# Performance work log

Measured on AMD Instinct MI355X. Metric: run time of the kernel, lower is better.

Reference implementation:

```python
import jax, jax.numpy as jnp
import numpy as np

N_NODES = 100000
N_HID = 128
N_ETYPES = 10
N_EDGES = 100000  # edges per etype


def setup_inputs() -> dict:
    key = jax.random.key(0)
    k1, k2, k3, k4 = jax.random.split(key, 4)
    h = jax.random.normal(k1, (N_NODES, N_HID), dtype=jnp.float32)
    W = jax.random.normal(k2, (N_ETYPES, N_HID), dtype=jnp.float32)
    src = jax.random.randint(k3, (N_ETYPES, N_EDGES), 0, N_NODES, dtype=jnp.int64)
    dst = jax.random.randint(k4, (N_ETYPES, N_EDGES), 0, N_NODES, dtype=jnp.int64)
    rel = jnp.arange(N_ETYPES, dtype=jnp.int64)  # rel2idx: etype -> relation row
    return {"h": h, "W": W, "src": src, "dst": dst, "rel": rel}


def reference(h, W, src, dst, rel):
    # DistMult: score(e) = sum_d h[src_e, d] * W[rel_e, d] * h[dst_e, d]
    h_u = h[src]          # [T, E, d]  gather src features
    h_v = h[dst]          # [T, E, d]  gather dst features
    h_r = W[rel]          # [T, d]     relation embedding per etype
    scores = jnp.einsum('ted,td,ted->te', h_u, h_r, h_v)  # [T, E]
    # pretrain_mode path applies sigmoid per etype
    return jax.nn.sigmoid(scores)
```

## Files before the change

### kernel.cpp

```cpp
#include <hip/hip_runtime.h>
#include <hip/hip_fp16.h>
#include <math.h>

#define N_NODES  100000
#define N_HID    128
#define N_ETYPES 10
#define N_EDGES  100000
#define TOT_EDGES (N_ETYPES * N_EDGES)

#define NSLICE    64
#define SLICE_CAP 16384
#define EPB_SC    2048

#define EDGES_PER_HW 4

typedef __attribute__((ext_vector_type(2))) _Float16 h2v;

#if defined(__has_builtin)
#if __has_builtin(__builtin_amdgcn_fdot2)
#define HAVE_FDOT2 1
#endif
#endif

__device__ __forceinline__ float dot2acc(h2v a, h2v b, float c) {
#ifdef HAVE_FDOT2
    return __builtin_amdgcn_fdot2(a, b, c, false);
#else
    return c + (float)a.x * (float)b.x + (float)a.y * (float)b.y;
#endif
}

template<int CTRL>
__device__ __forceinline__ float ror_add(float p) {
    int r = __builtin_amdgcn_update_dpp(0, __float_as_int(p), CTRL, 0xF, 0xF, true);
    return p + __int_as_float(r);
}
__device__ __forceinline__ float row16_sum(float p) {
    p = ror_add<0x121>(p);
    p = ror_add<0x122>(p);
    p = ror_add<0x124>(p);
    p = ror_add<0x128>(p);
    return p;
}

__device__ __forceinline__ float dot_row(uint4 a, uint4 b, uint4 w) {
    union { uint4 u; h2v p[4]; } ua, ub, uw;
    ua.u = a; ub.u = b; uw.u = w;
    float p = dot2acc(ua.p[0], (h2v)(uw.p[0] * ub.p[0]), 0.0f);
    p = dot2acc(ua.p[1], (h2v)(uw.p[1] * ub.p[1]), p);
    p = dot2acc(ua.p[2], (h2v)(uw.p[2] * ub.p[2]), p);
    p = dot2acc(ua.p[3], (h2v)(uw.p[3] * ub.p[3]), p);
    return p;
}

__global__ __launch_bounds__(256) void convert_kernel(
    const float* __restrict__ h, const float* __restrict__ W,
    const int*   __restrict__ rel,
    __half* __restrict__ h16, __half* __restrict__ Wr16,
    int* __restrict__ cursor)
{
    const size_t i = ((size_t)blockIdx.x * 256 + threadIdx.x) * 8;
    const float4 f0 = *(const float4*)(h + i);
    const float4 f1 = *(const float4*)(h + i + 4);
    union { uint4 u; __half2 p[4]; } pk;
    pk.p[0] = __floats2half2_rn(f0.x, f0.y);
    pk.p[1] = __floats2half2_rn(f0.z, f0.w);
    pk.p[2] = __floats2half2_rn(f1.x, f1.y);
    pk.p[3] = __floats2half2_rn(f1.z, f1.w);
    *(uint4*)(h16 + i) = pk.u;

    if (blockIdx.x == 0) {
        if (threadIdx.x < NSLICE) cursor[threadIdx.x] = threadIdx.x * SLICE_CAP;
        if (threadIdx.x < (N_ETYPES * N_HID / 8)) {
            const int j = threadIdx.x * 8;
            const int t = j >> 7;
            const int c = j & (N_HID - 1);
            const int r = rel[t];
            const float4 g0 = *(const float4*)(W + (size_t)r * N_HID + c);
            const float4 g1 = *(const float4*)(W + (size_t)r * N_HID + c + 4);
            union { uint4 u; __half2 p[4]; } pw;
            pw.p[0] = __floats2half2_rn(g0.x, g0.y);
            pw.p[1] = __floats2half2_rn(g0.z, g0.w);
            pw.p[2] = __floats2half2_rn(g1.x, g1.y);
            pw.p[3] = __floats2half2_rn(g1.z, g1.w);
            *(uint4*)(Wr16 + j) = pw.u;
        }
    }
}

__global__ __launch_bounds__(256) void scatter_kernel(
    const int* __restrict__ src, const int* __restrict__ dst,
    int* __restrict__ cursor, uint2* __restrict__ rec)
{
    __shared__ int lcnt[NSLICE];
    __shared__ int lbase[NSLICE];
    const int tid = threadIdx.x;
    if (tid < NSLICE) lcnt[tid] = 0;
    __syncthreads();

    const int e0 = blockIdx.x * EPB_SC + tid * 8;
    const bool active = (e0 < TOT_EDGES);

    int ss[8], dd[8], sl[8];
    if (active) {
        const int4 s0 = *(const int4*)(src + e0);
        const int4 s1 = *(const int4*)(src + e0 + 4);
        const int4 d0 = *(const int4*)(dst + e0);
        const int4 d1 = *(const int4*)(dst + e0 + 4);
        ss[0]=s0.x; ss[1]=s0.y; ss[2]=s0.z; ss[3]=s0.w;
        ss[4]=s1.x; ss[5]=s1.y; ss[6]=s1.z; ss[7]=s1.w;
        dd[0]=d0.x; dd[1]=d0.y; dd[2]=d0.z; dd[3]=d0.w;
        dd[4]=d1.x; dd[5]=d1.y; dd[6]=d1.z; dd[7]=d1.w;
        #pragma unroll
        for (int k = 0; k < 8; ++k) {
            sl[k] = (int)(((unsigned long long)(unsigned)dd[k] * 1407374884ULL) >> 41);
            atomicAdd(&lcnt[sl[k]], 1);
        }
    }
    __syncthreads();
    if (tid < NSLICE) {
        const int c = lcnt[tid];
        lbase[tid] = c ? atomicAdd(&cursor[tid], c) : 0;
        lcnt[tid] = 0;
    }
    __syncthreads();
    if (active) {
        #pragma unroll
        for (int k = 0; k < 8; ++k) {
            const int e   = e0 + k;
            const int ety = (int)(((unsigned long long)(unsigned)e * 1407374884ULL) >> 47);
            const int off = e - ety * N_EDGES;
            const int r   = atomicAdd(&lcnt[sl[k]], 1);
            const int pos = lbase[sl[k]] + r;
            const unsigned lo = (unsigned)ss[k] | ((unsigned)dd[k] << 17);
            const unsigned hi = ((unsigned)dd[k] >> 15) | ((unsigned)ety << 2) | ((unsigned)off << 6);
            rec[pos] = make_uint2(lo, hi);
        }
    }
}

__global__ __launch_bounds__(256) void score_kernel(
    const __half* __restrict__ h16,
    const __half* __restrict__ Wr16,
    const uint2*  __restrict__ rec,
    const int*    __restrict__ cursor,
    float*        __restrict__ out)
{
    const int tid  = threadIdx.x;
    const int lane = tid & 63;
    const int g    = lane >> 4;
    const int gl   = lane & 15;
    const int wid  = tid >> 6;

    const int b     = blockIdx.x;
    const int x     = b & 7;
    const int j     = b >> 3;
    const int s     = x + ((j >> 8) << 3);
    const int chunk = j & 255;
    const int sbase = s << 14;
    const int cnt   = cursor[s] - sbase;
    const int e_lo  = (chunk << 6) + (wid << 4);
    if (e_lo >= cnt) return;

    const unsigned col = (unsigned)gl << 3;

    const int i0 = e_lo + g;
    const int i1 = e_lo + 4 + g;
    const int i2 = e_lo + 8 + g;
    const int i3 = e_lo + 12 + g;
    const uint2 r0 = rec[sbase + (i0 < cnt ? i0 : 0)];
    const uint2 r1 = rec[sbase + (i1 < cnt ? i1 : 0)];
    const uint2 r2 = rec[sbase + (i2 < cnt ? i2 : 0)];
    const uint2 r3 = rec[sbase + (i3 < cnt ? i3 : 0)];

    const unsigned s0 = r0.x & 131071u, d0 = ((r0.x >> 17) | (r0.y << 15)) & 131071u;
    const unsigned t0 = (r0.y >> 2) & 15u,  o0 = r0.y >> 6;
    const unsigned s1 = r1.x & 131071u, d1 = ((r1.x >> 17) | (r1.y << 15)) & 131071u;
    const unsigned t1 = (r1.y >> 2) & 15u,  o1 = r1.y >> 6;
    const unsigned s2 = r2.x & 131071u, d2 = ((r2.x >> 17) | (r2.y << 15)) & 131071u;
    const unsigned t2 = (r2.y >> 2) & 15u,  o2 = r2.y >> 6;
    const unsigned s3 = r3.x & 131071u, d3 = ((r3.x >> 17) | (r3.y << 15)) & 131071u;
    const unsigned t3 = (r3.y >> 2) & 15u,  o3 = r3.y >> 6;

    const uint4 Wv0 = *(const uint4*)(Wr16 + ((t0 << 7) + col));
    const uint4 Wv1 = *(const uint4*)(Wr16 + ((t1 << 7) + col));
    const uint4 Wv2 = *(const uint4*)(Wr16 + ((t2 << 7) + col));
    const uint4 Wv3 = *(const uint4*)(Wr16 + ((t3 << 7) + col));
    const uint4 A0 = *(const uint4*)(h16 + ((s0 << 7) + col));
    const uint4 B0 = *(const uint4*)(h16 + ((d0 << 7) + col));
    const uint4 A1 = *(const uint4*)(h16 + ((s1 << 7) + col));
    const uint4 B1 = *(const uint4*)(h16 + ((d1 << 7) + col));
    const uint4 A2 = *(const uint4*)(h16 + ((s2 << 7) + col));
    const uint4 B2 = *(const uint4*)(h16 + ((d2 << 7) + col));
    const uint4 A3 = *(const uint4*)(h16 + ((s3 << 7) + col));
    const uint4 B3 = *(const uint4*)(h16 + ((d3 << 7) + col));

    float p0 = row16_sum(dot_row(A0, B0, Wv0));
    float p1 = row16_sum(dot_row(A1, B1, Wv1));
    float p2 = row16_sum(dot_row(A2, B2, Wv2));
    float p3 = row16_sum(dot_row(A3, B3, Wv3));

    if (gl < 4) {
        const int ii = e_lo + (gl << 2) + g;
        if (ii < cnt) {
            const float    res = (gl == 0) ? p0 : (gl == 1) ? p1 : (gl == 2) ? p2 : p3;
            const unsigned tt  = (gl == 0) ? t0 : (gl == 1) ? t1 : (gl == 2) ? t2 : t3;
            const unsigned oo  = (gl == 0) ? o0 : (gl == 1) ? o1 : (gl == 2) ? o2 : o3;
            out[tt * N_EDGES + oo] = 1.0f / (1.0f + __expf(-res));
        }
    }
}

__global__ __launch_bounds__(256) void convert_legacy_kernel(
    const float* __restrict__ h, const float* __restrict__ W,
    __half* __restrict__ h16, __half* __restrict__ W16)
{
    const size_t i = ((size_t)blockIdx.x * 256 + threadIdx.x) * 8;
    const float4 f0 = *(const float4*)(h + i);
    const float4 f1 = *(const float4*)(h + i + 4);
    union { uint4 u; __half2 p[4]; } pk;
    pk.p[0] = __floats2half2_rn(f0.x, f0.y);
    pk.p[1] = __floats2half2_rn(f0.z, f0.w);
    pk.p[2] = __floats2half2_rn(f1.x, f1.y);
    pk.p[3] = __floats2half2_rn(f1.z, f1.w);
    *(uint4*)(h16 + i) = pk.u;
    if (blockIdx.x == 0 && threadIdx.x < (N_ETYPES * N_HID / 8)) {
        const size_t j = (size_t)threadIdx.x * 8;
        const float4 g0 = *(const float4*)(W + j);
        const float4 g1 = *(const float4*)(W + j + 4);
        union { uint4 u; __half2 p[4]; } pw;
        pw.p[0] = __floats2half2_rn(g0.x, g0.y);
        pw.p[1] = __floats2half2_rn(g0.z, g0.w);
        pw.p[2] = __floats2half2_rn(g1.x, g1.y);
        pw.p[3] = __floats2half2_rn(g1.z, g1.w);
        *(uint4*)(W16 + j) = pw.u;
    }
}

__global__ __launch_bounds__(256) void distmult_score_f16_kernel(
    const __half* __restrict__ h16,
    const __half* __restrict__ W16,
    const int*    __restrict__ src,
    const int*    __restrict__ dst,
    const int*    __restrict__ rel,
    float*        __restrict__ out)
{
    const int t    = blockIdx.y;
    const int lane = threadIdx.x & 63;
    const int g    = lane >> 4;
    const int gl   = lane & 15;
    const int wid  = threadIdx.x >> 6;
    const int r = rel[t];
    union { uint4 u; h2v p[4]; } uw;
    uw.u = ((const uint4*)(W16 + (size_t)r * N_HID))[gl];
    const int base = t * N_EDGES;
    const int e0   = (blockIdx.x * 4 + wid) * 8;
    const int* sp = src + base + e0 + g;
    const int* dp = dst + base + e0 + g;
    const int s0 = sp[0], s1 = sp[4], d0 = dp[0], d1 = dp[4];
    const unsigned col = (unsigned)gl << 3;
    const uint4 A0 = *(const uint4*)(h16 + (((unsigned)s0 << 7) + col));
    const uint4 B0 = *(const uint4*)(h16 + (((unsigned)d0 << 7) + col));
    const uint4 A1 = *(const uint4*)(h16 + (((unsigned)s1 << 7) + col));
    const uint4 B1 = *(const uint4*)(h16 + (((unsigned)d1 << 7) + col));
    float p0 = row16_sum(dot_row(A0, B0, uw.u));
    float p1 = row16_sum(dot_row(A1, B1, uw.u));
    if (gl < 2) {
        const float res = gl ? p1 : p0;
        const int e = e0 + g + (gl << 2);
        out[base + e] = 1.0f / (1.0f + __expf(-res));
    }
}

__global__ __launch_bounds__(256) void distmult_score_f32_kernel(
    const float* __restrict__ h,
    const float* __restrict__ W,
    const int*   __restrict__ src,
    const int*   __restrict__ dst,
    const int*   __restrict__ rel,
    float*       __restrict__ out)
{
    const int t    = blockIdx.y;
    const int lane = threadIdx.x & 31;
    const int hw   = (blockIdx.x << 3) + (threadIdx.x >> 5);
    const int r = rel[t];
    const float4 w4 = ((const float4*)(W + (size_t)r * N_HID))[lane];
    const long base = (long)t * N_EDGES;
    const int  e0   = hw * EDGES_PER_HW;
    float res = 0.0f;
    #pragma unroll
    for (int k = 0; k < EDGES_PER_HW; ++k) {
        const int e = e0 + k;
        const int s = src[base + e];
        const int d = dst[base + e];
        const float4 a = ((const float4*)(h + (size_t)s * N_HID))[lane];
        const float4 b = ((const float4*)(h + (size_t)d * N_HID))[lane];
        float p = a.x * w4.x * b.x + a.y * w4.y * b.y
                + a.z * w4.z * b.z + a.w * w4.w * b.w;
        p += __shfl_xor(p, 16, 64);
        p += __shfl_xor(p, 8, 64);
        p += __shfl_xor(p, 4, 64);
        p += __shfl_xor(p, 2, 64);
        p += __shfl_xor(p, 1, 64);
        if (lane == k) res = p;
    }
    if (lane < EDGES_PER_HW) {
        out[base + e0 + lane] = 1.0f / (1.0f + __expf(-res));
    }
}

extern "C" void kernel_launch(void* const* d_in, const int* in_sizes, int n_in,
                              void* d_out, int out_size, void* d_ws, size_t ws_size,
                              hipStream_t stream) {
    const float* h   = (const float*)d_in[0];
    const float* W   = (const float*)d_in[1];
    const int*   src = (const int*)d_in[2];
    const int*   dst = (const int*)d_in[3];
    const int*   rel = (const int*)d_in[4];
    float*       out = (float*)d_out;

    const size_t h16_bytes  = (size_t)N_NODES * N_HID * sizeof(__half);
    const size_t wr16_bytes = 4096;
    const size_t rec_bytes  = (size_t)NSLICE * SLICE_CAP * 8;
    const size_t cur_bytes  = 4096;
    const size_t need_full  = h16_bytes + wr16_bytes + rec_bytes + cur_bytes;
    const size_t need_f16   = h16_bytes + (size_t)N_ETYPES * N_HID * sizeof(__half);

    if (ws_size >= need_full) {
        char* w = (char*)d_ws;
        __half* h16    = (__half*)w;   w += h16_bytes;
        __half* Wr16   = (__half*)w;   w += wr16_bytes;
        uint2*  rec    = (uint2*)w;    w += rec_bytes;
        int*    cursor = (int*)w;

        convert_kernel<<<(int)(((size_t)N_NODES * N_HID) / (256 * 8)), 256, 0, stream>>>(
            h, W, rel, h16, Wr16, cursor);
        scatter_kernel<<<(TOT_EDGES + EPB_SC - 1) / EPB_SC, 256, 0, stream>>>(
            src, dst, cursor, rec);
        score_kernel<<<NSLICE * (SLICE_CAP / 64), 256, 0, stream>>>(
            h16, Wr16, rec, cursor, out);
    } else if (ws_size >= need_f16) {
        __half* h16 = (__half*)d_ws;
        __half* W16 = h16 + (size_t)N_NODES * N_HID;
        convert_legacy_kernel<<<(int)(((size_t)N_NODES * N_HID) / (256 * 8)), 256, 0, stream>>>(
            h, W, h16, W16);
        dim3 grid(N_EDGES / 32, N_ETYPES);
        distmult_score_f16_kernel<<<grid, 256, 0, stream>>>(h16, W16, src, dst, rel, out);
    } else {
        dim3 grid(N_EDGES / (8 * EDGES_PER_HW), N_ETYPES);
        distmult_score_f32_kernel<<<grid, 256, 0, stream>>>(h, W, src, dst, rel, out);
    }
}
```

Baseline: 156.2 us.

## Fuse convert, scatter and score into one cooperative kernel with grid syncs

```diff
diff --git a/kernel.cpp b/kernel.cpp
--- a/kernel.cpp
+++ b/kernel.cpp
@@ -1,6 +1,9 @@
 #include <hip/hip_runtime.h>
+#include <hip/hip_cooperative_groups.h>
 #include <hip/hip_fp16.h>
 #include <math.h>
+
+namespace cg = cooperative_groups;
 
 #define N_NODES  100000
 #define N_HID    128
@@ -11,6 +14,9 @@
 #define NSLICE    64
 #define SLICE_CAP 16384
 #define EPB_SC    2048
+#define NBLK_SC   ((TOT_EDGES + EPB_SC - 1) / EPB_SC)
+#define NBFUSED   1024
+#define NVB_SCORE (NSLICE * (SLICE_CAP / 64))
 
 #define EDGES_PER_HW 4
 
@@ -53,52 +59,47 @@
     return p;
 }
 
-__global__ __launch_bounds__(256) void convert_kernel(
-    const float* __restrict__ h, const float* __restrict__ W,
-    const int*   __restrict__ rel,
-    __half* __restrict__ h16, __half* __restrict__ Wr16,
-    int* __restrict__ cursor)
-{
-    const size_t i = ((size_t)blockIdx.x * 256 + threadIdx.x) * 8;
-    const float4 f0 = *(const float4*)(h + i);
-    const float4 f1 = *(const float4*)(h + i + 4);
+
+__device__ __forceinline__ void conv_vec8(const float* __restrict__ h,
+                                          __half* __restrict__ h16, size_t off) {
+    const float4 f0 = *(const float4*)(h + off);
+    const float4 f1 = *(const float4*)(h + off + 4);
     union { uint4 u; __half2 p[4]; } pk;
     pk.p[0] = __floats2half2_rn(f0.x, f0.y);
     pk.p[1] = __floats2half2_rn(f0.z, f0.w);
     pk.p[2] = __floats2half2_rn(f1.x, f1.y);
     pk.p[3] = __floats2half2_rn(f1.z, f1.w);
-    *(uint4*)(h16 + i) = pk.u;
-
-    if (blockIdx.x == 0) {
-        if (threadIdx.x < NSLICE) cursor[threadIdx.x] = threadIdx.x * SLICE_CAP;
-        if (threadIdx.x < (N_ETYPES * N_HID / 8)) {
-            const int j = threadIdx.x * 8;
-            const int t = j >> 7;
-            const int c = j & (N_HID - 1);
-            const int r = rel[t];
-            const float4 g0 = *(const float4*)(W + (size_t)r * N_HID + c);
-            const float4 g1 = *(const float4*)(W + (size_t)r * N_HID + c + 4);
-            union { uint4 u; __half2 p[4]; } pw;
-            pw.p[0] = __floats2half2_rn(g0.x, g0.y);
-            pw.p[1] = __floats2half2_rn(g0.z, g0.w);
-            pw.p[2] = __floats2half2_rn(g1.x, g1.y);
-            pw.p[3] = __floats2half2_rn(g1.z, g1.w);
-            *(uint4*)(Wr16 + j) = pw.u;
-        }
-    }
-}
-
-__global__ __launch_bounds__(256) void scatter_kernel(
+    *(uint4*)(h16 + off) = pk.u;
+}
+
+__device__ __forceinline__ void wr16_and_cursor(int tid,
+    const float* __restrict__ W, const int* __restrict__ rel,
+    __half* __restrict__ Wr16, int* __restrict__ cursor) {
+    if (tid < NSLICE) cursor[tid] = tid * SLICE_CAP;
+    if (tid < (N_ETYPES * N_HID / 8)) {
+        const int j = tid * 8;
+        const int t = j >> 7;
+        const int c = j & (N_HID - 1);
+        const int r = rel[t];
+        const float4 g0 = *(const float4*)(W + (size_t)r * N_HID + c);
+        const float4 g1 = *(const float4*)(W + (size_t)r * N_HID + c + 4);
+        union { uint4 u; __half2 p[4]; } pw;
+        pw.p[0] = __floats2half2_rn(g0.x, g0.y);
+        pw.p[1] = __floats2half2_rn(g0.z, g0.w);
+        pw.p[2] = __floats2half2_rn(g1.x, g1.y);
+        pw.p[3] = __floats2half2_rn(g1.z, g1.w);
+        *(uint4*)(Wr16 + j) = pw.u;
+    }
+}
+
+__device__ __forceinline__ void scatter_block(int vb, int tid,
     const int* __restrict__ src, const int* __restrict__ dst,
-    int* __restrict__ cursor, uint2* __restrict__ rec)
-{
-    __shared__ int lcnt[NSLICE];
-    __shared__ int lbase[NSLICE];
-    const int tid = threadIdx.x;
+    int* __restrict__ cursor, uint2* __restrict__ rec,
+    int* lcnt, int* lbase) {
     if (tid < NSLICE) lcnt[tid] = 0;
     __syncthreads();
 
-    const int e0 = blockIdx.x * EPB_SC + tid * 8;
+    const int e0 = vb * EPB_SC + tid * 8;
     const bool active = (e0 < TOT_EDGES);
 
     int ss[8], dd[8], sl[8];
@@ -139,22 +140,17 @@
     }
 }
 
-__global__ __launch_bounds__(256) void score_kernel(
-    const __half* __restrict__ h16,
-    const __half* __restrict__ Wr16,
-    const uint2*  __restrict__ rec,
-    const int*    __restrict__ cursor,
-    float*        __restrict__ out)
-{
-    const int tid  = threadIdx.x;
+__device__ __forceinline__ void score_vblock(int vb, int tid,
+    const __half* __restrict__ h16, const __half* __restrict__ Wr16,
+    const uint2* __restrict__ rec, const int* __restrict__ cursor,
+    float* __restrict__ out) {
     const int lane = tid & 63;
     const int g    = lane >> 4;
     const int gl   = lane & 15;
     const int wid  = tid >> 6;
 
-    const int b     = blockIdx.x;
-    const int x     = b & 7;
-    const int j     = b >> 3;
+    const int x     = vb & 7;
+    const int j     = vb >> 3;
     const int s     = x + ((j >> 8) << 3);
     const int chunk = j & 255;
     const int sbase = s << 14;
@@ -211,65 +207,63 @@
     }
 }
 
-__global__ __launch_bounds__(256) void convert_legacy_kernel(
+__global__ __launch_bounds__(256, 4) void fused_kernel(
     const float* __restrict__ h, const float* __restrict__ W,
-    __half* __restrict__ h16, __half* __restrict__ W16)
-{
-    const size_t i = ((size_t)blockIdx.x * 256 + threadIdx.x) * 8;
-    const float4 f0 = *(const float4*)(h + i);
-    const float4 f1 = *(const float4*)(h + i + 4);
-    union { uint4 u; __half2 p[4]; } pk;
-    pk.p[0] = __floats2half2_rn(f0.x, f0.y);
-    pk.p[1] = __floats2half2_rn(f0.z, f0.w);
-    pk.p[2] = __floats2half2_rn(f1.x, f1.y);
-    pk.p[3] = __floats2half2_rn(f1.z, f1.w);
-    *(uint4*)(h16 + i) = pk.u;
-    if (blockIdx.x == 0 && threadIdx.x < (N_ETYPES * N_HID / 8)) {
-        const size_t j = (size_t)threadIdx.x * 8;
-        const float4 g0 = *(const float4*)(W + j);
-        const float4 g1 = *(const float4*)(W + j + 4);
-        union { uint4 u; __half2 p[4]; } pw;
-        pw.p[0] = __floats2half2_rn(g0.x, g0.y);
-        pw.p[1] = __floats2half2_rn(g0.z, g0.w);
-        pw.p[2] = __floats2half2_rn(g1.x, g1.y);
-        pw.p[3] = __floats2half2_rn(g1.z, g1.w);
-        *(uint4*)(W16 + j) = pw.u;
-    }
-}
-
-__global__ __launch_bounds__(256) void distmult_score_f16_kernel(
+    const int*   __restrict__ rel,
+    const int*   __restrict__ src, const int* __restrict__ dst,
+    __half* __restrict__ h16, __half* __restrict__ Wr16,
+    uint2* __restrict__ rec, int* __restrict__ cursor,
+    float* __restrict__ out)
+{
+    __shared__ int lcnt[NSLICE];
+    __shared__ int lbase[NSLICE];
+    cg::grid_group grid = cg::this_grid();
+    const int b   = blockIdx.x;
+    const int tid = threadIdx.x;
+    const int nth = NBFUSED * 256;
+
+    const int totvec = (N_NODES * N_HID) / 8;
+    for (int i = b * 256 + tid; i < totvec; i += nth)
+        conv_vec8(h, h16, (size_t)i * 8);
+    if (b == 0) wr16_and_cursor(tid, W, rel, Wr16, cursor);
+    grid.sync();
+
+    if (b < NBLK_SC)
+        scatter_block(b, tid, src, dst, cursor, rec, lcnt, lbase);
+    grid.sync();
+
+    #pragma unroll 1
+    for (int k = 0; k < NVB_SCORE / NBFUSED; ++k)
+        score_vblock(b + k * NBFUSED, tid, h16, Wr16, rec, cursor, out);
+}
+
+__global__ __launch_bounds__(256) void convert_kernel(
+    const float* __restrict__ h, const float* __restrict__ W,
+    const int*   __restrict__ rel,
+    __half* __restrict__ h16, __half* __restrict__ Wr16,
+    int* __restrict__ cursor)
+{
+    conv_vec8(h, h16, ((size_t)blockIdx.x * 256 + threadIdx.x) * 8);
+    if (blockIdx.x == 0) wr16_and_cursor(threadIdx.x, W, rel, Wr16, cursor);
+}
+
+__global__ __launch_bounds__(256) void scatter_kernel(
+    const int* __restrict__ src, const int* __restrict__ dst,
+    int* __restrict__ cursor, uint2* __restrict__ rec)
+{
+    __shared__ int lcnt[NSLICE];
+    __shared__ int lbase[NSLICE];
+    scatter_block(blockIdx.x, threadIdx.x, src, dst, cursor, rec, lcnt, lbase);
+}
+
+__global__ __launch_bounds__(256) void score_kernel(
     const __half* __restrict__ h16,
-    const __half* __restrict__ W16,
-    const int*    __restrict__ src,
-    const int*    __restrict__ dst,
-    const int*    __restrict__ rel,
+    const __half* __restrict__ Wr16,
+    const uint2*  __restrict__ rec,
+    const int*    __restrict__ cursor,
     float*        __restrict__ out)
 {
-    const int t    = blockIdx.y;
-    const int lane = threadIdx.x & 63;
-    const int g    = lane >> 4;
-    const int gl   = lane & 15;
-    const int wid  = threadIdx.x >> 6;
-    const int r = rel[t];
-    union { uint4 u; h2v p[4]; } uw;
-    uw.u = ((const uint4*)(W16 + (size_t)r * N_HID))[gl];
-    const int base = t * N_EDGES;
-    const int e0   = (blockIdx.x * 4 + wid) * 8;
-    const int* sp = src + base + e0 + g;
-    const int* dp = dst + base + e0 + g;
-    const int s0 = sp[0], s1 = sp[4], d0 = dp[0], d1 = dp[4];
-    const unsigned col = (unsigned)gl << 3;
-    const uint4 A0 = *(const uint4*)(h16 + (((unsigned)s0 << 7) + col));
-    const uint4 B0 = *(const uint4*)(h16 + (((unsigned)d0 << 7) + col));
-    const uint4 A1 = *(const uint4*)(h16 + (((unsigned)s1 << 7) + col));
-    const uint4 B1 = *(const uint4*)(h16 + (((unsigned)d1 << 7) + col));
-    float p0 = row16_sum(dot_row(A0, B0, uw.u));
-    float p1 = row16_sum(dot_row(A1, B1, uw.u));
-    if (gl < 2) {
-        const float res = gl ? p1 : p0;
-        const int e = e0 + g + (gl << 2);
-        out[base + e] = 1.0f / (1.0f + __expf(-res));
-    }
+    score_vblock(blockIdx.x, threadIdx.x, h16, Wr16, rec, cursor, out);
 }
 
 __global__ __launch_bounds__(256) void distmult_score_f32_kernel(
@@ -324,7 +318,6 @@
     const size_t rec_bytes  = (size_t)NSLICE * SLICE_CAP * 8;
     const size_t cur_bytes  = 4096;
     const size_t need_full  = h16_bytes + wr16_bytes + rec_bytes + cur_bytes;
-    const size_t need_f16   = h16_bytes + (size_t)N_ETYPES * N_HID * sizeof(__half);
 
     if (ws_size >= need_full) {
         char* w = (char*)d_ws;
@@ -333,19 +326,17 @@
         uint2*  rec    = (uint2*)w;    w += rec_bytes;
         int*    cursor = (int*)w;
 
+        void* kargs[] = { (void*)&h, (void*)&W, (void*)&rel, (void*)&src, (void*)&dst,
+                          (void*)&h16, (void*)&Wr16, (void*)&rec, (void*)&cursor, (void*)&out };
+        hipError_t err = hipLaunchCooperativeKernel(
+            (const void*)fused_kernel, dim3(NBFUSED), dim3(256), kargs, 0, stream);
+        if (err == hipSuccess) return;
+        (void)hipGetLastError();
+
         convert_kernel<<<(int)(((size_t)N_NODES * N_HID) / (256 * 8)), 256, 0, stream>>>(
             h, W, rel, h16, Wr16, cursor);
-        scatter_kernel<<<(TOT_EDGES + EPB_SC - 1) / EPB_SC, 256, 0, stream>>>(
-            src, dst, cursor, rec);
-        score_kernel<<<NSLICE * (SLICE_CAP / 64), 256, 0, stream>>>(
-            h16, Wr16, rec, cursor, out);
-    } else if (ws_size >= need_f16) {
-        __half* h16 = (__half*)d_ws;
-        __half* W16 = h16 + (size_t)N_NODES * N_HID;
-        convert_legacy_kernel<<<(int)(((size_t)N_NODES * N_HID) / (256 * 8)), 256, 0, stream>>>(
-            h, W, h16, W16);
-        dim3 grid(N_EDGES / 32, N_ETYPES);
-        distmult_score_f16_kernel<<<grid, 256, 0, stream>>>(h16, W16, src, dst, rel, out);
+        scatter_kernel<<<NBLK_SC, 256, 0, stream>>>(src, dst, cursor, rec);
+        score_kernel<<<NVB_SCORE, 256, 0, stream>>>(h16, Wr16, rec, cursor, out);
     } else {
         dim3 grid(N_EDGES / (8 * EDGES_PER_HW), N_ETYPES);
         distmult_score_f32_kernel<<<grid, 256, 0, stream>>>(h, W, src, dst, rel, out);
```

New measurement: 384.5 us. 2.46x slower.
